# Kernel tuning notes

Measured on AMD Instinct MI355X. Metric: run time of the kernel, lower is better.

Reference implementation:

```python
import jax, jax.numpy as jnp
import numpy as np

N_BLOCKS = 5
D_HIDDEN = 512
D_LATENT = 512
NUM_FREQ = 10
IMG_H = IMG_W = 128


@jax.custom_vjp
def trunc_exp(x):
    return jnp.exp(x)

def _te_fwd(x):
    return jnp.exp(x), x

def _te_bwd(x, g):
    return (g * jnp.exp(jnp.clip(x, -15.0, 15.0)),)

trunc_exp.defvjp(_te_fwd, _te_bwd)


def setup_inputs() -> dict:
    key = jax.random.key(0)
    ks = jax.random.split(key, 12)
    cam, ray, samp = 2, 1024, 48
    world_xyz = jax.random.normal(ks[0], (cam, ray, samp, 3), jnp.float32) * 0.5
    world_xyz = world_xyz.at[..., 2].add(2.5)  # keep points in front of identity camera
    c2w = jnp.tile(jnp.eye(4, dtype=jnp.float32), (cam, 1, 1))
    k_mat = jnp.tile(jnp.array([[128.0, 0.0, 64.0], [0.0, 128.0, 64.0], [0.0, 0.0, 1.0]], jnp.float32), (cam, 1, 1))
    features = jax.random.normal(ks[1], (cam, D_LATENT, IMG_H, IMG_W), jnp.float32)
    s = 0.02
    d_in = 3 + 3 * 2 * NUM_FREQ  # 63
    return {
        'world_xyz': world_xyz,
        'c2w': c2w,
        'k_mat': k_mat,
        'features': features,
        'lin_in_w': jax.random.normal(ks[2], (d_in, D_HIDDEN), jnp.float32) * s,
        'lin_in_b': jnp.zeros((D_HIDDEN,), jnp.float32),
        'lin_z_w': jax.random.normal(ks[3], (N_BLOCKS, D_LATENT, D_HIDDEN), jnp.float32) * s,
        'lin_z_b': jnp.zeros((N_BLOCKS, D_HIDDEN), jnp.float32),
        'fc0_w': jax.random.normal(ks[4], (N_BLOCKS, D_HIDDEN, D_HIDDEN), jnp.float32) * s,
        'fc0_b': jnp.zeros((N_BLOCKS, D_HIDDEN), jnp.float32),
        'fc1_w': jax.random.normal(ks[5], (N_BLOCKS, D_HIDDEN, D_HIDDEN), jnp.float32) * s,
        'fc1_b': jnp.zeros((N_BLOCKS, D_HIDDEN), jnp.float32),
        'lin_out_w': jax.random.normal(ks[6], (D_HIDDEN, 1), jnp.float32) * s,
        'lin_out_b': jnp.zeros((1,), jnp.float32),
    }


def _bilinear(feat, uv):
    # feat: [C, H, W]; uv: [N, 2] pixel coords. Bilinear, border padding, align_corners=True.
    Hd, Wd = feat.shape[1], feat.shape[2]
    x = jnp.clip(uv[:, 0], 0.0, Wd - 1.0)
    y = jnp.clip(uv[:, 1], 0.0, Hd - 1.0)
    x0 = jnp.floor(x); y0 = jnp.floor(y)
    x0i = x0.astype(jnp.int32); y0i = y0.astype(jnp.int32)
    x1i = jnp.minimum(x0i + 1, Wd - 1); y1i = jnp.minimum(y0i + 1, Hd - 1)
    wx = x - x0; wy = y - y0
    f00 = feat[:, y0i, x0i]; f01 = feat[:, y0i, x1i]
    f10 = feat[:, y1i, x0i]; f11 = feat[:, y1i, x1i]
    out = (f00 * ((1 - wx) * (1 - wy)) + f01 * (wx * (1 - wy)) +
           f10 * ((1 - wx) * wy) + f11 * (wx * wy))
    return out.T  # [N, C]


def _forward(world_xyz, c2w, k_mat, features, lin_in_w, lin_in_b, lin_z_w, lin_z_b,
             fc0_w, fc0_b, fc1_w, fc1_b, lin_out_w, lin_out_b):
    B, R, S, _ = world_xyz.shape
    pts = world_xyz.reshape(B, R * S, 3)
    # world -> camera (w2c = inverse of rigid c2w)
    rot = c2w[:, :3, :3]
    trans = c2w[:, :3, 3]
    cam_xyz = jnp.einsum('bji,bnj->bni', rot, pts - trans[:, None])  # R^T (p - t)
    # project with intrinsics
    uvw = jnp.einsum('bij,bnj->bni', k_mat, cam_xyz)
    z = uvw[..., 2:3]
    z = jnp.where(jnp.abs(z) < 1e-6, 1e-6, z)
    uv = uvw[..., :2] / z  # [B, N, 2] pixel coords
    aligned = jax.vmap(_bilinear)(features, uv)  # [B, N, C]
    # NeRF positional encoding (include_input=True, freqs 2^0..2^9, scaled by 2*pi)
    freqs = 2.0 ** jnp.arange(NUM_FREQ, dtype=jnp.float32)
    scaled = (2.0 * jnp.pi) * cam_xyz[..., None] * freqs  # [B, N, 3, F]
    scaled = scaled.reshape(B, R * S, 3 * NUM_FREQ)
    enc = jnp.concatenate([cam_xyz, jnp.sin(scaled), jnp.cos(scaled)], axis=-1)  # [B, N, 63]
    # ResnetFC: lin_in then residual blocks with latent injection
    h = enc @ lin_in_w + lin_in_b
    for i in range(N_BLOCKS):
        h = h + aligned @ lin_z_w[i] + lin_z_b[i]
        net = jax.nn.relu(h) @ fc0_w[i] + fc0_b[i]
        dx = jax.nn.relu(net) @ fc1_w[i] + fc1_b[i]
        h = h + dx
    sigma = jax.nn.relu(h) @ lin_out_w + lin_out_b  # [B, N, 1]
    return trunc_exp(sigma).reshape(B, R, S, 1)


def reference(world_xyz, c2w, k_mat, features, lin_in_w, lin_in_b, lin_z_w, lin_z_b,
              fc0_w, fc0_b, fc1_w, fc1_b, lin_out_w, lin_out_b):
    return _forward(world_xyz, c2w, k_mat, features, lin_in_w, lin_in_b, lin_z_w, lin_z_b,
                    fc0_w, fc0_b, fc1_w, fc1_b, lin_out_w, lin_out_b)
```

## Files before the change

kernel.cpp:

```cpp
#include <hip/hip_runtime.h>

typedef __bf16 bf16_t;
typedef bf16_t bf16x8 __attribute__((ext_vector_type(8)));
typedef float f32x4 __attribute__((ext_vector_type(4)));
typedef unsigned short u16;

#define P_TOTAL 98304
#define PTS_PER_BATCH 49152
#define PITCH 520

__device__ __forceinline__ u16 f2bs(float f){ bf16_t b=(bf16_t)f; return __builtin_bit_cast(u16,b); }

__device__ __forceinline__ void bar_lds(){
  asm volatile("s_waitcnt lgkmcnt(0)" ::: "memory");
  __builtin_amdgcn_s_barrier();
  __builtin_amdgcn_sched_barrier(0);
}

__global__ void k_wtrans15(const float* __restrict__ lz, const float* __restrict__ f0,
                           const float* __restrict__ f1, u16* __restrict__ dst){
  int kt = blockIdx.x, ns = blockIdx.y, z = blockIdx.z;
  const float* src = (z<5) ? (lz + (size_t)z*262144)
                   : (z<10 ? (f0 + (size_t)(z-5)*262144)
                           : (f1 + (size_t)(z-10)*262144));
  u16* d = dst + (size_t)z*262144 + (size_t)(ns*16 + kt)*1024;
  int l = threadIdx.x;
  int col = ns*32 + (l&15);
  int kr  = kt*32 + (l>>4)*8;
  #pragma unroll
  for (int nt=0;nt<2;nt++){
    bf16x8 o;
    #pragma unroll
    for (int j=0;j<8;j++) o[j] = (bf16_t)src[(size_t)(kr+j)*512 + col + nt*16];
    *(bf16x8*)(d + nt*512 + l*8) = o;
  }
}

__global__ void k_wtrans_in(const float* __restrict__ w, u16* __restrict__ dst){
  int kt = blockIdx.x, ns = blockIdx.y;
  u16* d = dst + (size_t)(ns*2 + kt)*1024;
  int l = threadIdx.x;
  int col = ns*32 + (l&15);
  int kr  = kt*32 + (l>>4)*8;
  #pragma unroll
  for (int nt=0;nt<2;nt++){
    bf16x8 o;
    #pragma unroll
    for (int j=0;j<8;j++){
      int k = kr + j;
      o[j] = (k < 63) ? (bf16_t)w[(size_t)k*512 + col + nt*16] : (bf16_t)0.f;
    }
    *(bf16x8*)(d + nt*512 + l*8) = o;
  }
}

__global__ void k_featT(const float* __restrict__ feat, u16* __restrict__ featT){
  int x = threadIdx.x;
  int c8 = blockIdx.x*8;
  int y = blockIdx.y, b = blockIdx.z;
  float v[8];
  #pragma unroll
  for (int j=0;j<8;j++)
    v[j] = feat[(((size_t)(b*512 + c8 + j))*128 + y)*128 + x];
  bf16x8 o;
  #pragma unroll
  for (int j=0;j<8;j++) o[j] = (bf16_t)v[j];
  *(bf16x8*)(featT + (((size_t)(b*128 + y))*128 + x)*512 + c8) = o;
}

__global__ void k_points(const float* __restrict__ world, const float* __restrict__ c2w,
                         const float* __restrict__ kmat, const u16* __restrict__ featT,
                         u16* __restrict__ alignedB, u16* __restrict__ encB){
  int wid = threadIdx.x >> 6, lane = threadIdx.x & 63;
  int gp = blockIdx.x*4 + wid;
  int b = gp / PTS_PER_BATCH;
  const float* wp = world + (size_t)gp*3;
  float px = wp[0], py = wp[1], pz = wp[2];
  const float* cw = c2w + b*16;
  float dx = px - cw[3], dy = py - cw[7], dz = pz - cw[11];
  float cx = cw[0]*dx + cw[4]*dy + cw[8]*dz;
  float cy = cw[1]*dx + cw[5]*dy + cw[9]*dz;
  float cz = cw[2]*dx + cw[6]*dy + cw[10]*dz;
  const float* km = kmat + b*9;
  float u0 = km[0]*cx + km[1]*cy + km[2]*cz;
  float v0 = km[3]*cx + km[4]*cy + km[5]*cz;
  float zz = km[6]*cx + km[7]*cy + km[8]*cz;
  if (fabsf(zz) < 1e-6f) zz = 1e-6f;
  float uu = u0/zz, vv = v0/zz;
  float xf = fminf(fmaxf(uu, 0.f), 127.f);
  float yf = fminf(fmaxf(vv, 0.f), 127.f);
  float x0f = floorf(xf), y0f = floorf(yf);
  int x0 = (int)x0f, y0 = (int)y0f;
  int x1 = min(x0+1,127), y1 = min(y0+1,127);
  float wx = xf - x0f, wy = yf - y0f;
  float w00 = (1.f-wx)*(1.f-wy), w01 = wx*(1.f-wy), w10 = (1.f-wx)*wy, w11 = wx*wy;
  size_t fb = (size_t)b*128*128*512;
  int c8 = lane*8;
  const bf16x8 t00 = *(const bf16x8*)(featT + fb + (size_t)(y0*128+x0)*512 + c8);
  const bf16x8 t01 = *(const bf16x8*)(featT + fb + (size_t)(y0*128+x1)*512 + c8);
  const bf16x8 t10 = *(const bf16x8*)(featT + fb + (size_t)(y1*128+x0)*512 + c8);
  const bf16x8 t11 = *(const bf16x8*)(featT + fb + (size_t)(y1*128+x1)*512 + c8);
  bf16x8 o;
  #pragma unroll
  for (int j=0;j<8;j++){
    float r = (float)t00[j]*w00 + (float)t01[j]*w01 + (float)t10[j]*w10 + (float)t11[j]*w11;
    o[j] = (bf16_t)r;
  }
  *(bf16x8*)(alignedB + (size_t)gp*512 + c8) = o;
  float cam[3] = {cx, cy, cz};
  float e;
  if (lane < 3) e = cam[lane];
  else if (lane < 33){
    int i = (lane-3)/10, f = (lane-3)%10;
    e = sinf(6.2831855f * cam[i] * (float)(1<<f));
  } else if (lane < 63){
    int i = (lane-33)/10, f = (lane-33)%10;
    e = cosf(6.2831855f * cam[i] * (float)(1<<f));
  } else e = 0.f;
  encB[(size_t)gp*64 + lane] = f2bs(e);
}


#define MFMA_BF16 __builtin_amdgcn_mfma_f32_16x16x32_bf16

template<int NK>
__device__ __forceinline__ void gemm2(const u16* sB, const u16* __restrict__ apS,
                                      const u16* __restrict__ apN,
                                      int fm, int fk8, f32x4 (&acc)[4][4], bf16x8 (&a)[2][4]){
  const u16* bp = sB + fm*PITCH + fk8*8;
  bf16x8 br[2][4];
  #pragma unroll
  for (int bt=0; bt<4; ++bt) br[0][bt] = *(const bf16x8*)(bp + bt*16*PITCH);
  #pragma unroll 1
  for (int kb=0; kb<NK/2-1; ++kb){
    #pragma unroll
    for (int d=0; d<2; ++d){
      const int kt = kb*2 + d;
      #pragma unroll
      for (int bt=0; bt<4; ++bt)
        br[d^1][bt] = *(const bf16x8*)(bp + bt*16*PITCH + (kt+1)*32);
      bf16x8 ac0=a[d][0], ac1=a[d][1], ac2=a[d][2], ac3=a[d][3];
      #pragma unroll
      for (int nt=0; nt<4; ++nt)
        a[d][nt] = *(const bf16x8*)(apS + (nt>>1)*(NK*1024) + (kt+2)*1024 + (nt&1)*512);
      #pragma unroll
      for (int bt=0; bt<4; ++bt){
        acc[bt][0] = MFMA_BF16(ac0, br[d][bt], acc[bt][0], 0,0,0);
        acc[bt][1] = MFMA_BF16(ac1, br[d][bt], acc[bt][1], 0,0,0);
        acc[bt][2] = MFMA_BF16(ac2, br[d][bt], acc[bt][2], 0,0,0);
        acc[bt][3] = MFMA_BF16(ac3, br[d][bt], acc[bt][3], 0,0,0);
      }
    }
  }
  #pragma unroll
  for (int d=0; d<2; ++d){
    if (d == 0){
      #pragma unroll
      for (int bt=0; bt<4; ++bt)
        br[1][bt] = *(const bf16x8*)(bp + bt*16*PITCH + (NK-1)*32);
    }
    bf16x8 ac0=a[d][0], ac1=a[d][1], ac2=a[d][2], ac3=a[d][3];
    #pragma unroll
    for (int nt=0; nt<4; ++nt)
      a[d][nt] = *(const bf16x8*)(apN + (nt>>1)*16384 + d*1024 + (nt&1)*512);
    #pragma unroll
    for (int bt=0; bt<4; ++bt){
      acc[bt][0] = MFMA_BF16(ac0, br[d][bt], acc[bt][0], 0,0,0);
      acc[bt][1] = MFMA_BF16(ac1, br[d][bt], acc[bt][1], 0,0,0);
      acc[bt][2] = MFMA_BF16(ac2, br[d][bt], acc[bt][2], 0,0,0);
      acc[bt][3] = MFMA_BF16(ac3, br[d][bt], acc[bt][3], 0,0,0);
    }
  }
}

__device__ __forceinline__ void add_bias2(const float* __restrict__ bias, int wn64, int rq,
                                          f32x4 (&acc)[4][4]){
  #pragma unroll
  for (int nt=0; nt<4; ++nt){
    f32x4 bv = *(const f32x4*)&bias[wn64 + nt*16 + rq];
    #pragma unroll
    for (int bt=0; bt<4; ++bt)
      #pragma unroll
      for (int r=0; r<4; ++r)
        acc[bt][nt][r] += bv[r];
  }
}

__device__ __forceinline__ void write_relu2(u16* dst, int fm, int rq, int wn64,
                                            f32x4 (&acc)[4][4]){
  #pragma unroll
  for (int bt=0; bt<4; ++bt){
    int m = bt*16 + fm;
    #pragma unroll
    for (int nt=0; nt<4; ++nt){
      int kb = wn64 + nt*16 + rq;
      u16 p0 = f2bs(fmaxf(acc[bt][nt][0], 0.f));
      u16 p1 = f2bs(fmaxf(acc[bt][nt][1], 0.f));
      u16 p2 = f2bs(fmaxf(acc[bt][nt][2], 0.f));
      u16 p3 = f2bs(fmaxf(acc[bt][nt][3], 0.f));
      uint2 v;
      v.x = (unsigned)p0 | ((unsigned)p1 << 16);
      v.y = (unsigned)p2 | ((unsigned)p3 << 16);
      *(uint2*)&dst[m*PITCH + kb] = v;
    }
  }
}

__global__ __launch_bounds__(512, 2) void k_net(
    const u16* __restrict__ alignedB, const u16* __restrict__ encB,
    const u16* __restrict__ wtin, const float* __restrict__ b_in,
    const u16* __restrict__ wts, const float* __restrict__ bz,
    const float* __restrict__ b0, const float* __restrict__ b1,
    const float* __restrict__ wout, const float* __restrict__ bout,
    float* __restrict__ out)
{
  __shared__ u16 bufA[64*PITCH];
  __shared__ u16 bufB[64*PITCH];
  const int t = threadIdx.x, w = t>>6, l = t&63;
  const int m0 = blockIdx.x*64;
  const int wn64 = w*64, fm = l&15, fk8 = l>>4, rq = (l>>4)*4;

  const u16* apE = wtin + (size_t)w*4096 + l*8;
  bf16x8 afr[2][4];
  #pragma unroll
  for (int d=0; d<2; ++d)
    #pragma unroll
    for (int nt=0; nt<4; ++nt)
      afr[d][nt] = *(const bf16x8*)(apE + (nt>>1)*2048 + d*1024 + (nt&1)*512);

  {
    int m = t>>3, c = t&7;
    #pragma unroll
    for (int j=0;j<8;j++){
      int kc = c + j*8;
      *(uint4*)&bufA[m*PITCH + kc*8] =
          *(const uint4*)(alignedB + (size_t)(m0+m)*512 + kc*8);
    }
  }
  {
    int m = t>>3, kc = t&7;
    *(uint4*)&bufB[m*PITCH + kc*8] =
        *(const uint4*)(encB + (size_t)(m0+m)*64 + kc*8);
  }
  bar_lds();

  const u16* apz0 = wts + (size_t)w*32768 + l*8;
  f32x4 h[4][4] = {};
  gemm2<2>(bufB, apE, apz0, fm, fk8, h, afr);
  add_bias2(b_in, wn64, rq, h);

  #pragma unroll 1
  for (int i=0;i<5;i++){
    const u16* apz  = wts + (size_t)i*262144      + (size_t)w*32768 + l*8;
    const u16* apf0 = wts + (size_t)(5+i)*262144  + (size_t)w*32768 + l*8;
    const u16* apf1 = wts + (size_t)(10+i)*262144 + (size_t)w*32768 + l*8;
    const u16* apzn = (i<4) ? (wts + (size_t)(i+1)*262144 + (size_t)w*32768 + l*8) : apE;

    gemm2<16>(bufA, apz, apf0, fm, fk8, h, afr);
    add_bias2(bz + i*512, wn64, rq, h);
    bar_lds();
    write_relu2(bufB, fm, rq, wn64, h);
    bar_lds();
    f32x4 acc[4][4] = {};
    gemm2<16>(bufB, apf0, apf1, fm, fk8, acc, afr);
    add_bias2(b0 + i*512, wn64, rq, acc);
    bar_lds();
    write_relu2(bufB, fm, rq, wn64, acc);
    bar_lds();
    gemm2<16>(bufB, apf1, apzn, fm, fk8, h, afr);
    add_bias2(b1 + i*512, wn64, rq, h);
  }

  float s[4];
  {
    #pragma unroll
    for (int bt=0; bt<4; ++bt) s[bt] = 0.f;
    #pragma unroll
    for (int nt=0; nt<4; ++nt){
      f32x4 wv = *(const f32x4*)&wout[wn64 + nt*16 + rq];
      #pragma unroll
      for (int bt=0; bt<4; ++bt)
        #pragma unroll
        for (int r=0; r<4; ++r)
          s[bt] += fmaxf(h[bt][nt][r], 0.f) * wv[r];
    }
  }
  #pragma unroll
  for (int bt=0; bt<4; ++bt){
    s[bt] += __shfl_xor(s[bt], 16, 64);
    s[bt] += __shfl_xor(s[bt], 32, 64);
  }
  bar_lds();
  float* red = (float*)bufB;
  if (l < 16){
    #pragma unroll
    for (int bt=0; bt<4; ++bt)
      red[w*64 + bt*16 + l] = s[bt];
  }
  bar_lds();
  if (t < 64){
    float a = bout[0];
    #pragma unroll
    for (int wv=0; wv<8; wv++) a += red[wv*64 + t];
    out[m0 + t] = expf(a);
  }
}

extern "C" void kernel_launch(void* const* d_in, const int* in_sizes, int n_in,
                              void* d_out, int out_size, void* d_ws, size_t ws_size,
                              hipStream_t stream) {
  const float* world = (const float*)d_in[0];
  const float* c2w   = (const float*)d_in[1];
  const float* kmat  = (const float*)d_in[2];
  const float* feat  = (const float*)d_in[3];
  const float* w_in  = (const float*)d_in[4];
  const float* b_in  = (const float*)d_in[5];
  const float* w_z   = (const float*)d_in[6];
  const float* b_z   = (const float*)d_in[7];
  const float* w_f0  = (const float*)d_in[8];
  const float* b_f0  = (const float*)d_in[9];
  const float* w_f1  = (const float*)d_in[10];
  const float* b_f1  = (const float*)d_in[11];
  const float* w_out = (const float*)d_in[12];
  const float* b_out = (const float*)d_in[13];
  float* out = (float*)d_out;
  char* ws = (char*)d_ws;

  size_t off = 0;
  u16* wts   = (u16*)(ws + off); off += (size_t)15*262144*2;
  u16* wtin  = (u16*)(ws + off); off += (size_t)512*64*2;
  u16* featT = (u16*)(ws + off); off += (size_t)2*128*128*512*2;
  u16* alignedB = (u16*)(ws + off); off += (size_t)P_TOTAL*512*2;
  u16* encB  = (u16*)(ws + off); off += (size_t)P_TOTAL*64*2;

  k_wtrans15<<<dim3(16,16,15), 64, 0, stream>>>(w_z, w_f0, w_f1, wts);
  k_wtrans_in<<<dim3(2,16,1), 64, 0, stream>>>(w_in, wtin);
  k_featT<<<dim3(64,128,2), 128, 0, stream>>>(feat, featT);
  k_points<<<dim3(P_TOTAL/4), 256, 0, stream>>>(world, c2w, kmat, featT, alignedB, encB);
  k_net<<<dim3(P_TOTAL/64), 512, 0, stream>>>(alignedB, encB, wtin, b_in, wts,
      b_z, b_f0, b_f1, w_out, b_out, out);
}
```

Before: 837.3 us.

## Store activations in MFMA fragment order to remove padded LDS layout

k_points now handles 16 points per block and stages aligned features and encodings in LDS. It then writes them to global memory pre-swizzled into MFMA B-fragment order. k_net copies these tiles linearly into LDS and reads B fragments contiguously. write_relu3 writes in the same fragment layout, the padded PITCH rows are dropped, and MFMAs are issued before the next weight-fragment loads. The goal is conflict-free, contiguous LDS access and simpler global loads, at the cost of an extra LDS staging pass and barrier in k_points and fragment-layout indexing that must stay exactly right.

```diff
diff --git a/kernel.cpp b/kernel.cpp
--- a/kernel.cpp
+++ b/kernel.cpp
@@ -7,7 +7,6 @@
 
 #define P_TOTAL 98304
 #define PTS_PER_BATCH 49152
-#define PITCH 520
 
 __device__ __forceinline__ u16 f2bs(float f){ bf16_t b=(bf16_t)f; return __builtin_bit_cast(u16,b); }
 
@@ -68,11 +67,15 @@
   *(bf16x8*)(featT + (((size_t)(b*128 + y))*128 + x)*512 + c8) = o;
 }
 
-__global__ void k_points(const float* __restrict__ world, const float* __restrict__ c2w,
-                         const float* __restrict__ kmat, const u16* __restrict__ featT,
-                         u16* __restrict__ alignedB, u16* __restrict__ encB){
+__global__ __launch_bounds__(1024) void k_points(
+    const float* __restrict__ world, const float* __restrict__ c2w,
+    const float* __restrict__ kmat, const u16* __restrict__ featT,
+    u16* __restrict__ alignedF, u16* __restrict__ encF){
+  __shared__ u16 act[16*520];
+  __shared__ u16 encs[16*72];
   int wid = threadIdx.x >> 6, lane = threadIdx.x & 63;
-  int gp = blockIdx.x*4 + wid;
+  int p0 = blockIdx.x*16;
+  int gp = p0 + wid;
   int b = gp / PTS_PER_BATCH;
   const float* wp = world + (size_t)gp*3;
   float px = wp[0], py = wp[1], pz = wp[2];
@@ -106,7 +109,7 @@
     float r = (float)t00[j]*w00 + (float)t01[j]*w01 + (float)t10[j]*w10 + (float)t11[j]*w11;
     o[j] = (bf16_t)r;
   }
-  *(bf16x8*)(alignedB + (size_t)gp*512 + c8) = o;
+  *(bf16x8*)&act[wid*520 + lane*8] = o;
   float cam[3] = {cx, cy, cz};
   float e;
   if (lane < 3) e = cam[lane];
@@ -117,20 +120,34 @@
     int i = (lane-33)/10, f = (lane-33)%10;
     e = cosf(6.2831855f * cam[i] * (float)(1<<f));
   } else e = 0.f;
-  encB[(size_t)gp*64 + lane] = f2bs(e);
+  encs[wid*72 + lane] = f2bs(e);
+  __syncthreads();
+  int t = threadIdx.x;
+  int g = blockIdx.x & 3;
+  size_t blk = (size_t)(blockIdx.x >> 2);
+  {
+    int kt = t>>6, lo = t&63, fm = lo&15, fk8 = lo>>4;
+    bf16x8 v = *(const bf16x8*)&act[fm*520 + kt*32 + fk8*8];
+    *(bf16x8*)(alignedF + blk*32768 + (size_t)(kt*4+g)*512 + lo*8) = v;
+  }
+  if (t < 128){
+    int kt = t>>6, lo = t&63, fm = lo&15, fk8 = lo>>4;
+    bf16x8 v = *(const bf16x8*)&encs[fm*72 + kt*32 + fk8*8];
+    *(bf16x8*)(encF + blk*4096 + (size_t)(kt*4+g)*512 + lo*8) = v;
+  }
 }
 
 
 #define MFMA_BF16 __builtin_amdgcn_mfma_f32_16x16x32_bf16
 
 template<int NK>
-__device__ __forceinline__ void gemm2(const u16* sB, const u16* __restrict__ apS,
+__device__ __forceinline__ void gemm3(const u16* sB, const u16* __restrict__ apS,
                                       const u16* __restrict__ apN,
-                                      int fm, int fk8, f32x4 (&acc)[4][4], bf16x8 (&a)[2][4]){
-  const u16* bp = sB + fm*PITCH + fk8*8;
+                                      int l, f32x4 (&acc)[4][4], bf16x8 (&a)[2][4]){
+  const u16* bp = sB + l*8;
   bf16x8 br[2][4];
   #pragma unroll
-  for (int bt=0; bt<4; ++bt) br[0][bt] = *(const bf16x8*)(bp + bt*16*PITCH);
+  for (int bt=0; bt<4; ++bt) br[0][bt] = *(const bf16x8*)(bp + bt*512);
   #pragma unroll 1
   for (int kb=0; kb<NK/2-1; ++kb){
     #pragma unroll
@@ -138,18 +155,17 @@
       const int kt = kb*2 + d;
       #pragma unroll
       for (int bt=0; bt<4; ++bt)
-        br[d^1][bt] = *(const bf16x8*)(bp + bt*16*PITCH + (kt+1)*32);
-      bf16x8 ac0=a[d][0], ac1=a[d][1], ac2=a[d][2], ac3=a[d][3];
+        br[d^1][bt] = *(const bf16x8*)(bp + (kt+1)*2048 + bt*512);
+      #pragma unroll
+      for (int bt=0; bt<4; ++bt){
+        acc[bt][0] = MFMA_BF16(a[d][0], br[d][bt], acc[bt][0], 0,0,0);
+        acc[bt][1] = MFMA_BF16(a[d][1], br[d][bt], acc[bt][1], 0,0,0);
+        acc[bt][2] = MFMA_BF16(a[d][2], br[d][bt], acc[bt][2], 0,0,0);
+        acc[bt][3] = MFMA_BF16(a[d][3], br[d][bt], acc[bt][3], 0,0,0);
+      }
       #pragma unroll
       for (int nt=0; nt<4; ++nt)
         a[d][nt] = *(const bf16x8*)(apS + (nt>>1)*(NK*1024) + (kt+2)*1024 + (nt&1)*512);
-      #pragma unroll
-      for (int bt=0; bt<4; ++bt){
-        acc[bt][0] = MFMA_BF16(ac0, br[d][bt], acc[bt][0], 0,0,0);
-        acc[bt][1] = MFMA_BF16(ac1, br[d][bt], acc[bt][1], 0,0,0);
-        acc[bt][2] = MFMA_BF16(ac2, br[d][bt], acc[bt][2], 0,0,0);
-        acc[bt][3] = MFMA_BF16(ac3, br[d][bt], acc[bt][3], 0,0,0);
-      }
     }
   }
   #pragma unroll
@@ -157,19 +173,18 @@
     if (d == 0){
       #pragma unroll
       for (int bt=0; bt<4; ++bt)
-        br[1][bt] = *(const bf16x8*)(bp + bt*16*PITCH + (NK-1)*32);
-    }
-    bf16x8 ac0=a[d][0], ac1=a[d][1], ac2=a[d][2], ac3=a[d][3];
+        br[1][bt] = *(const bf16x8*)(bp + (NK-1)*2048 + bt*512);
+    }
+    #pragma unroll
+    for (int bt=0; bt<4; ++bt){
+      acc[bt][0] = MFMA_BF16(a[d][0], br[d][bt], acc[bt][0], 0,0,0);
+      acc[bt][1] = MFMA_BF16(a[d][1], br[d][bt], acc[bt][1], 0,0,0);
+      acc[bt][2] = MFMA_BF16(a[d][2], br[d][bt], acc[bt][2], 0,0,0);
+      acc[bt][3] = MFMA_BF16(a[d][3], br[d][bt], acc[bt][3], 0,0,0);
+    }
     #pragma unroll
     for (int nt=0; nt<4; ++nt)
       a[d][nt] = *(const bf16x8*)(apN + (nt>>1)*16384 + d*1024 + (nt&1)*512);
-    #pragma unroll
-    for (int bt=0; bt<4; ++bt){
-      acc[bt][0] = MFMA_BF16(ac0, br[d][bt], acc[bt][0], 0,0,0);
-      acc[bt][1] = MFMA_BF16(ac1, br[d][bt], acc[bt][1], 0,0,0);
-      acc[bt][2] = MFMA_BF16(ac2, br[d][bt], acc[bt][2], 0,0,0);
-      acc[bt][3] = MFMA_BF16(ac3, br[d][bt], acc[bt][3], 0,0,0);
-    }
   }
 }
 
@@ -186,14 +201,13 @@
   }
 }
 
-__device__ __forceinline__ void write_relu2(u16* dst, int fm, int rq, int wn64,
+__device__ __forceinline__ void write_relu3(u16* dst, int w, int fm, int fk8,
                                             f32x4 (&acc)[4][4]){
-  #pragma unroll
-  for (int bt=0; bt<4; ++bt){
-    int m = bt*16 + fm;
+  u16* base = dst + w*4096 + (fk8>>1)*128 + fm*8 + (fk8&1)*4;
+  #pragma unroll
+  for (int bt=0; bt<4; ++bt)
     #pragma unroll
     for (int nt=0; nt<4; ++nt){
-      int kb = wn64 + nt*16 + rq;
       u16 p0 = f2bs(fmaxf(acc[bt][nt][0], 0.f));
       u16 p1 = f2bs(fmaxf(acc[bt][nt][1], 0.f));
       u16 p2 = f2bs(fmaxf(acc[bt][nt][2], 0.f));
@@ -201,24 +215,28 @@
       uint2 v;
       v.x = (unsigned)p0 | ((unsigned)p1 << 16);
       v.y = (unsigned)p2 | ((unsigned)p3 << 16);
-      *(uint2*)&dst[m*PITCH + kb] = v;
-    }
-  }
+      *(uint2*)(base + (nt>>1)*2048 + (nt&1)*256 + bt*512) = v;
+    }
 }
 
 __global__ __launch_bounds__(512, 2) void k_net(
-    const u16* __restrict__ alignedB, const u16* __restrict__ encB,
+    const u16* __restrict__ alignedF, const u16* __restrict__ encF,
     const u16* __restrict__ wtin, const float* __restrict__ b_in,
     const u16* __restrict__ wts, const float* __restrict__ bz,
     const float* __restrict__ b0, const float* __restrict__ b1,
     const float* __restrict__ wout, const float* __restrict__ bout,
     float* __restrict__ out)
 {
-  __shared__ u16 bufA[64*PITCH];
-  __shared__ u16 bufB[64*PITCH];
+  __shared__ u16 bufA[32768];
+  __shared__ u16 bufB[32768];
   const int t = threadIdx.x, w = t>>6, l = t&63;
-  const int m0 = blockIdx.x*64;
   const int wn64 = w*64, fm = l&15, fk8 = l>>4, rq = (l>>4)*4;
+
+  uint4 sa[8];
+  const uint4* srcA = (const uint4*)(alignedF + (size_t)blockIdx.x*32768);
+  #pragma unroll
+  for (int j=0;j<8;j++) sa[j] = srcA[j*512 + t];
+  uint4 sb = *((const uint4*)(encF + (size_t)blockIdx.x*4096) + t);
 
   const u16* apE = wtin + (size_t)w*4096 + l*8;
   bf16x8 afr[2][4];
@@ -228,25 +246,14 @@
     for (int nt=0; nt<4; ++nt)
       afr[d][nt] = *(const bf16x8*)(apE + (nt>>1)*2048 + d*1024 + (nt&1)*512);
 
-  {
-    int m = t>>3, c = t&7;
-    #pragma unroll
-    for (int j=0;j<8;j++){
-      int kc = c + j*8;
-      *(uint4*)&bufA[m*PITCH + kc*8] =
-          *(const uint4*)(alignedB + (size_t)(m0+m)*512 + kc*8);
-    }
-  }
-  {
-    int m = t>>3, kc = t&7;
-    *(uint4*)&bufB[m*PITCH + kc*8] =
-        *(const uint4*)(encB + (size_t)(m0+m)*64 + kc*8);
-  }
+  #pragma unroll
+  for (int j=0;j<8;j++) *((uint4*)bufA + j*512 + t) = sa[j];
+  *((uint4*)bufB + t) = sb;
   bar_lds();
 
   const u16* apz0 = wts + (size_t)w*32768 + l*8;
   f32x4 h[4][4] = {};
-  gemm2<2>(bufB, apE, apz0, fm, fk8, h, afr);
+  gemm3<2>(bufB, apE, apz0, l, h, afr);
   add_bias2(b_in, wn64, rq, h);
 
   #pragma unroll 1
@@ -256,18 +263,18 @@
     const u16* apf1 = wts + (size_t)(10+i)*262144 + (size_t)w*32768 + l*8;
     const u16* apzn = (i<4) ? (wts + (size_t)(i+1)*262144 + (size_t)w*32768 + l*8) : apE;
 
-    gemm2<16>(bufA, apz, apf0, fm, fk8, h, afr);
+    gemm3<16>(bufA, apz, apf0, l, h, afr);
     add_bias2(bz + i*512, wn64, rq, h);
     bar_lds();
-    write_relu2(bufB, fm, rq, wn64, h);
+    write_relu3(bufB, w, fm, fk8, h);
     bar_lds();
     f32x4 acc[4][4] = {};
-    gemm2<16>(bufB, apf0, apf1, fm, fk8, acc, afr);
+    gemm3<16>(bufB, apf0, apf1, l, acc, afr);
     add_bias2(b0 + i*512, wn64, rq, acc);
     bar_lds();
-    write_relu2(bufB, fm, rq, wn64, acc);
+    write_relu3(bufB, w, fm, fk8, acc);
     bar_lds();
-    gemm2<16>(bufB, apf1, apzn, fm, fk8, h, afr);
+    gemm3<16>(bufB, apf1, apzn, l, h, afr);
     add_bias2(b1 + i*512, wn64, rq, h);
   }
 
@@ -302,7 +309,7 @@
     float a = bout[0];
     #pragma unroll
     for (int wv=0; wv<8; wv++) a += red[wv*64 + t];
-    out[m0 + t] = expf(a);
+    out[blockIdx.x*64 + t] = expf(a);
   }
 }
 
@@ -330,13 +337,13 @@
   u16* wts   = (u16*)(ws + off); off += (size_t)15*262144*2;
   u16* wtin  = (u16*)(ws + off); off += (size_t)512*64*2;
   u16* featT = (u16*)(ws + off); off += (size_t)2*128*128*512*2;
-  u16* alignedB = (u16*)(ws + off); off += (size_t)P_TOTAL*512*2;
-  u16* encB  = (u16*)(ws + off); off += (size_t)P_TOTAL*64*2;
+  u16* alignedF = (u16*)(ws + off); off += (size_t)P_TOTAL*512*2;
+  u16* encF  = (u16*)(ws + off); off += (size_t)P_TOTAL*64*2;
 
   k_wtrans15<<<dim3(16,16,15), 64, 0, stream>>>(w_z, w_f0, w_f1, wts);
   k_wtrans_in<<<dim3(2,16,1), 64, 0, stream>>>(w_in, wtin);
   k_featT<<<dim3(64,128,2), 128, 0, stream>>>(feat, featT);
-  k_points<<<dim3(P_TOTAL/4), 256, 0, stream>>>(world, c2w, kmat, featT, alignedB, encB);
-  k_net<<<dim3(P_TOTAL/64), 512, 0, stream>>>(alignedB, encB, wtin, b_in, wts,
+  k_points<<<dim3(P_TOTAL/16), 1024, 0, stream>>>(world, c2w, kmat, featT, alignedF, encF);
+  k_net<<<dim3(P_TOTAL/64), 512, 0, stream>>>(alignedF, encF, wtin, b_in, wts,
       b_z, b_f0, b_f1, w_out, b_out, out);
 }
```

Result: no change. 839.5 us (+0.3%).
